# Optimization experiments

Hardware: AMD Instinct MI355X
Metric: run time of the kernel (lower is better)

Reference implementation:

```python
import jax, jax.numpy as jnp
import numpy as np


def setup_inputs() -> dict:
    key = jax.random.key(0)
    k1, k2 = jax.random.split(key)
    B, C, H, W = 2, 32, 128, 256
    left = jax.random.normal(k1, (B, C, H, W), dtype=jnp.float32)
    right = jax.random.normal(k2, (B, C, H, W), dtype=jnp.float32)
    return {"left": left, "right": right, "max_disp": 32}


def reference(left, right, max_disp):
    # left, right: [B, C, H, W] -> cost volume [B, 2C, D, H, W]
    B, C, H, W = left.shape
    d = jnp.arange(max_disp)          # [D]
    w = jnp.arange(W)                 # [W]
    # left slice for disparity d: left[..., w+d], zero where w+d >= W
    pos_l = w[None, :] + d[:, None]   # [D, W]
    mask_l = pos_l < W
    # right slice for disparity d: right[..., w-d], zero where w < d
    pos_r = w[None, :] - d[:, None]   # [D, W]
    mask_r = pos_r >= 0
    # gather along W: [B, C, H, D, W]
    lg = jnp.take(left, jnp.clip(pos_l, 0, W - 1), axis=-1)
    rg = jnp.take(right, jnp.clip(pos_r, 0, W - 1), axis=-1)
    lg = jnp.where(mask_l, lg, jnp.zeros((), left.dtype))
    rg = jnp.where(mask_r, rg, jnp.zeros((), right.dtype))
    # -> [B, C, D, H, W]
    lg = lg.transpose(0, 1, 3, 2, 4)
    rg = rg.transpose(0, 1, 3, 2, 4)
    return jnp.concatenate([lg, rg], axis=1)  # [B, 2C, D, H, W]
```

## Files before the change

### kernel.cpp

```cpp
#include <hip/hip_runtime.h>


typedef float vfloat4 __attribute__((ext_vector_type(4)));

__global__ __launch_bounds__(256) void costvol_kernel(
        const float* __restrict__ left,
        const float* __restrict__ right,
        float* __restrict__ out) {
    constexpr int W4 = 64, H = 128, D = 32, C = 32;

    const unsigned tid = threadIdx.x;
    const unsigned w4  = tid & 63u;
    const unsigned hlo = tid >> 6;
    const unsigned bid = blockIdx.x;
    const unsigned h   = (bid & 31u) * 4u + hlo;
    const unsigned c   = (bid >> 5) & 31u;
    const unsigned b   = bid >> 10;

    const size_t inoff = ((size_t)(b * C + c) * H + h) * 256;
    const vfloat4* lrow = reinterpret_cast<const vfloat4*>(left  + inoff);
    const vfloat4* rrow = reinterpret_cast<const vfloat4*>(right + inoff);

    const size_t dstride = (size_t)W4 * H;
    vfloat4* outL = reinterpret_cast<vfloat4*>(out)
                  + (size_t)w4
                  + (size_t)W4 * ((size_t)h + (size_t)H * D * ((size_t)c + 2u * C * (size_t)b));
    vfloat4* outR = outL + (size_t)C * D * dstride;

    const vfloat4 zero4 = {0.f, 0.f, 0.f, 0.f};

    float l[36];
#pragma unroll
    for (int k = 0; k < 9; ++k) {
        vfloat4 v = (w4 + (unsigned)k < (unsigned)W4) ? lrow[w4 + k] : zero4;
        l[4*k+0] = v.x; l[4*k+1] = v.y; l[4*k+2] = v.z; l[4*k+3] = v.w;
    }
#pragma unroll
    for (int d = 0; d < D; ++d) {
        vfloat4 q = { l[d], l[d+1], l[d+2], l[d+3] };
        outL[(size_t)d * dstride] = q;
    }

    float r[36];
#pragma unroll
    for (int m = 0; m < 9; ++m) {
        vfloat4 v = (w4 + (unsigned)m >= 8u) ? rrow[(int)(w4 + m) - 8] : zero4;
        r[4*m+0] = v.x; r[4*m+1] = v.y; r[4*m+2] = v.z; r[4*m+3] = v.w;
    }
#pragma unroll
    for (int d = 0; d < D; ++d) {
        vfloat4 q = { r[32-d], r[33-d], r[34-d], r[35-d] };
        outR[(size_t)d * dstride] = q;
    }
}

extern "C" void kernel_launch(void* const* d_in, const int* in_sizes, int n_in,
                              void* d_out, int out_size, void* d_ws, size_t ws_size,
                              hipStream_t stream) {
    const float* left  = (const float*)d_in[0];
    const float* right = (const float*)d_in[1];
    float* out = (float*)d_out;

    costvol_kernel<<<2048, 256, 0, stream>>>(left, right, out);
}
```

Before: 540.4 us.

## Assign each block one disparity-channel slab for contiguous output writes

Restructures the work split so each block produces one contiguous (batch, channel, disparity) output slab across all rows, instead of each thread loading an input row once and scattering 32 disparity outputs. Inputs are now gathered per element with clamped indices and masks, and each input row is re-read once per disparity. The intent is fully sequential write streams and more blocks in flight, at the cost of many more input reads, which rely on cache hits.

```diff
diff --git a/kernel.cpp b/kernel.cpp
--- a/kernel.cpp
+++ b/kernel.cpp
@@ -7,50 +7,44 @@
         const float* __restrict__ left,
         const float* __restrict__ right,
         float* __restrict__ out) {
-    constexpr int W4 = 64, H = 128, D = 32, C = 32;
+    constexpr int W = 256, H = 128, C = 32;
 
     const unsigned tid = threadIdx.x;
     const unsigned w4  = tid & 63u;
     const unsigned hlo = tid >> 6;
+
     const unsigned bid = blockIdx.x;
-    const unsigned h   = (bid & 31u) * 4u + hlo;
-    const unsigned c   = (bid >> 5) & 31u;
-    const unsigned b   = bid >> 10;
+    const unsigned d   = bid & 31u;
+    const unsigned c2  = (bid >> 5) & 63u;
+    const unsigned b   = bid >> 11;
 
-    const size_t inoff = ((size_t)(b * C + c) * H + h) * 256;
-    const vfloat4* lrow = reinterpret_cast<const vfloat4*>(left  + inoff);
-    const vfloat4* rrow = reinterpret_cast<const vfloat4*>(right + inoff);
+    const bool     isL = (c2 < (unsigned)C);
+    const unsigned c   = isL ? c2 : (c2 - (unsigned)C);
+    const float*   src = isL ? left : right;
 
-    const size_t dstride = (size_t)W4 * H;
-    vfloat4* outL = reinterpret_cast<vfloat4*>(out)
-                  + (size_t)w4
-                  + (size_t)W4 * ((size_t)h + (size_t)H * D * ((size_t)c + 2u * C * (size_t)b));
-    vfloat4* outR = outL + (size_t)C * D * dstride;
+    const float* row0 = src + ((size_t)(b * C + c) * H + hlo) * W;
 
-    const vfloat4 zero4 = {0.f, 0.f, 0.f, 0.f};
-
-    float l[36];
+    const int base = isL ? (int)(4u * w4 + d) : (int)(4u * w4) - (int)d;
+    int  idx[4];
+    bool msk[4];
 #pragma unroll
-    for (int k = 0; k < 9; ++k) {
-        vfloat4 v = (w4 + (unsigned)k < (unsigned)W4) ? lrow[w4 + k] : zero4;
-        l[4*k+0] = v.x; l[4*k+1] = v.y; l[4*k+2] = v.z; l[4*k+3] = v.w;
-    }
-#pragma unroll
-    for (int d = 0; d < D; ++d) {
-        vfloat4 q = { l[d], l[d+1], l[d+2], l[d+3] };
-        outL[(size_t)d * dstride] = q;
+    for (int j = 0; j < 4; ++j) {
+        int t = base + j;
+        msk[j] = isL ? (t < W) : (t >= 0);
+        idx[j] = t < 0 ? 0 : (t > W - 1 ? W - 1 : t);
     }
 
-    float r[36];
+    vfloat4* o = reinterpret_cast<vfloat4*>(out) + (size_t)bid * 8192u + tid;
+
 #pragma unroll
-    for (int m = 0; m < 9; ++m) {
-        vfloat4 v = (w4 + (unsigned)m >= 8u) ? rrow[(int)(w4 + m) - 8] : zero4;
-        r[4*m+0] = v.x; r[4*m+1] = v.y; r[4*m+2] = v.z; r[4*m+3] = v.w;
-    }
-#pragma unroll
-    for (int d = 0; d < D; ++d) {
-        vfloat4 q = { r[32-d], r[33-d], r[34-d], r[35-d] };
-        outR[(size_t)d * dstride] = q;
+    for (int it = 0; it < 32; ++it) {
+        const float* row = row0 + (size_t)it * (4u * W);
+        vfloat4 v;
+        v.x = msk[0] ? row[idx[0]] : 0.f;
+        v.y = msk[1] ? row[idx[1]] : 0.f;
+        v.z = msk[2] ? row[idx[2]] : 0.f;
+        v.w = msk[3] ? row[idx[3]] : 0.f;
+        o[(size_t)it * 256u] = v;
     }
 }
 
@@ -61,5 +55,5 @@
     const float* right = (const float*)d_in[1];
     float* out = (float*)d_out;
 
-    costvol_kernel<<<2048, 256, 0, stream>>>(left, right, out);
+    costvol_kernel<<<4096, 256, 0, stream>>>(left, right, out);
 }
```

Measured after the change: 639.3 us. +18.3%, slower.
